# Kernel tuning notes

Measured on AMD Instinct MI355X. Metric: run time of the kernel, lower is better.

Reference implementation:

```python
import jax, jax.numpy as jnp
import numpy as np

N, E, H, FE, DIM = 50000, 800000, 128, 16, 3
MF = 2 * H + FE + 1  # message_features: 2*hidden + edge_feats + radial (e3, not relaxed)


def _lin(key, fan_in, fan_out):
    return jax.random.normal(key, (fan_in, fan_out), jnp.float32) / np.sqrt(fan_in)


def setup_inputs() -> dict:
    key = jax.random.key(0)
    ks = jax.random.split(key, 16)
    inp = {
        "h": jax.random.normal(ks[0], (N, H), jnp.float32),
        "coords": jax.random.normal(ks[1], (N, DIM), jnp.float32),
        "a": jax.random.normal(ks[2], (E, FE), jnp.float32),
        "src": jax.random.randint(ks[3], (E,), 0, N),
        "dst": jax.random.randint(ks[4], (E,), 0, N),
        # coord_mlp: Lin(MF,H)+silu, Lin(H,H)+silu, Lin(H,1,bias=False) w/ gain 0.001
        "wc1": _lin(ks[5], MF, H), "bc1": jnp.zeros((H,), jnp.float32),
        "wc2": _lin(ks[6], H, H), "bc2": jnp.zeros((H,), jnp.float32),
        "wc3": _lin(ks[7], H, 1) * 0.001,
        # edge_mlp: Lin(MF,H)+silu, Lin(H,H)+silu
        "we1": _lin(ks[8], MF, H), "be1": jnp.zeros((H,), jnp.float32),
        "we2": _lin(ks[9], H, H), "be2": jnp.zeros((H,), jnp.float32),
        # att_mlp: Lin(H,1)+sigmoid
        "wa": _lin(ks[10], H, 1), "ba": jnp.zeros((1,), jnp.float32),
        # node_mlp: Lin(2H,H)+silu, Lin(H,H)
        "wn1": _lin(ks[11], 2 * H, H), "bn1": jnp.zeros((H,), jnp.float32),
        "wn2": _lin(ks[12], H, H), "bn2": jnp.zeros((H,), jnp.float32),
    }
    return inp


def reference(h, coords, a, src, dst,
              wc1, bc1, wc2, bc2, wc3,
              we1, be1, we2, be2,
              wa, ba, wn1, bn1, wn2, bn2):
    silu = jax.nn.silu
    # --- edge gather ---
    hs, hd = h[src], h[dst]              # [E, H]
    xs, xd = coords[src], coords[dst]    # [E, 3]
    diffs = xs - xd                      # [E, 3]
    radials = jnp.sum(diffs * diffs, axis=-1, keepdims=True)  # [E, 1]
    f = jnp.concatenate([hs, hd, radials, a], axis=-1)        # [E, MF]
    # --- coord message ---
    c = silu(f @ wc1 + bc1)
    c = silu(c @ wc2 + bc2)
    scale = c @ wc3                      # [E, 1]
    msg_x = scale * diffs / (radials + 1.0)                   # [E, 3]
    # --- hidden message with attention gate ---
    m = silu(f @ we1 + be1)
    m = silu(m @ we2 + be2)              # [E, H]
    msg_h = jax.nn.sigmoid(m @ wa + ba) * m                   # [E, H]
    # --- scatter-sum to destination nodes ---
    x_agg = jax.ops.segment_sum(msg_x, dst, num_segments=N)   # [N, 3]
    h_agg = jax.ops.segment_sum(msg_h, dst, num_segments=N)   # [N, H]
    coords_out = coords + x_agg
    n = silu(jnp.concatenate([h, h_agg], axis=-1) @ wn1 + bn1)
    h_out = h + (n @ wn2 + bn2)
    return (h_out, coords_out)
```

## Files before the change

kernel.cpp:

```cpp
#include <hip/hip_runtime.h>

#define NN 50000
#define NE 800000
#define HD 128
#define FED 16
#define MFD 273
#define K1 288
#define NO1 256
#define FSTR 296
#define NFSTR 264
#define NNSTR 136

typedef __bf16 bf16x8 __attribute__((ext_vector_type(8)));
typedef float f32x4 __attribute__((ext_vector_type(4)));
typedef unsigned short u16;

__device__ __forceinline__ u16 f2b(float x) {
  unsigned u = __builtin_bit_cast(unsigned, x);
  return (u16)((u + 0x7FFFu + ((u >> 16) & 1u)) >> 16);
}
__device__ __forceinline__ float siluf(float x) { return x / (1.f + __expf(-x)); }

__global__ void pack_weights(const float* __restrict__ wc1, const float* __restrict__ we1,
                             const float* __restrict__ wc2, const float* __restrict__ we2,
                             const float* __restrict__ wn1, const float* __restrict__ wn2,
                             u16* __restrict__ W1t, u16* __restrict__ W2ct,
                             u16* __restrict__ W2mt, u16* __restrict__ Wn1t,
                             u16* __restrict__ Wn2t) {
  int i = blockIdx.x * 256 + threadIdx.x;
  if (i < 256 * K1) {
    int n = i / K1, k = i - n * K1;
    float v = 0.f;
    if (k < MFD) v = (n < HD) ? wc1[k * HD + n] : we1[k * HD + (n - HD)];
    W1t[i] = f2b(v);
    return;
  }
  int j = i - 256 * K1;
  if (j < HD * HD) {
    int n = j >> 7, k = j & 127;
    W2ct[j] = f2b(wc2[k * HD + n]);
    W2mt[j] = f2b(we2[k * HD + n]);
    return;
  }
  j -= HD * HD;
  if (j < HD * 256) {
    int n = j >> 8, k = j & 255;
    Wn1t[j] = f2b(wn1[k * HD + n]);
    return;
  }
  j -= HD * 256;
  if (j < HD * HD) {
    int n = j >> 7, k = j & 127;
    Wn2t[j] = f2b(wn2[k * HD + n]);
  }
}

__global__ __launch_bounds__(256, 2) void edge_kernel(
    const float* __restrict__ h, const float* __restrict__ coords,
    const float* __restrict__ a, const int* __restrict__ src,
    const int* __restrict__ dst,
    const float* __restrict__ bc1, const float* __restrict__ be1,
    const float* __restrict__ bc2, const float* __restrict__ be2,
    const float* __restrict__ wc3, const float* __restrict__ wa,
    const float* __restrict__ ba,
    const u16* __restrict__ W1t, const u16* __restrict__ W2ct,
    const u16* __restrict__ W2mt,
    float* __restrict__ x_agg, float* __restrict__ h_agg) {
  __shared__ u16 fL[128 * FSTR];
  __shared__ float diffL[128][3];
  __shared__ float radL[128];
  __shared__ int dstL[128];

  const int tid = threadIdx.x;
  const int wave = tid >> 6;
  const int lane = tid & 63;
  const int wrow = wave * 32;
  const int ebase = blockIdx.x * 128;

  {
    const int r = wrow + (lane >> 1);
    const int q = lane & 1;
    const int e = ebase + r;
    const int s = src[e];
    const int d = dst[e];
    const float4* hs4 = (const float4*)(h + (size_t)s * HD) + q * 16;
    const float4* hd4 = (const float4*)(h + (size_t)d * HD) + q * 16;
    u16* frow = &fL[r * FSTR];
#pragma unroll
    for (int u = 0; u < 16; ++u) {
      float4 v = hs4[u];
      ushort4 b; b.x = f2b(v.x); b.y = f2b(v.y); b.z = f2b(v.z); b.w = f2b(v.w);
      *(ushort4*)(frow + q * 64 + u * 4) = b;
    }
#pragma unroll
    for (int u = 0; u < 16; ++u) {
      float4 v = hd4[u];
      ushort4 b; b.x = f2b(v.x); b.y = f2b(v.y); b.z = f2b(v.z); b.w = f2b(v.w);
      *(ushort4*)(frow + HD + q * 64 + u * 4) = b;
    }
    if (q == 0) {
      float dx = coords[(size_t)s * 3 + 0] - coords[(size_t)d * 3 + 0];
      float dy = coords[(size_t)s * 3 + 1] - coords[(size_t)d * 3 + 1];
      float dz = coords[(size_t)s * 3 + 2] - coords[(size_t)d * 3 + 2];
      float rad = dx * dx + dy * dy + dz * dz;
      diffL[r][0] = dx; diffL[r][1] = dy; diffL[r][2] = dz;
      radL[r] = rad; dstL[r] = d;
      frow[256] = f2b(rad);
    } else {
      const float* ap = a + (size_t)e * FED;
#pragma unroll
      for (int u = 0; u < FED; ++u) frow[257 + u] = f2b(ap[u]);
#pragma unroll
      for (int u = MFD; u < K1; ++u) frow[u] = 0;
    }
  }

  const int ln = lane & 15;
  const int khi = lane >> 4;

  bf16x8 a1[2][9];
#pragma unroll
  for (int st = 0; st < 2; ++st)
#pragma unroll
    for (int kk = 0; kk < 9; ++kk)
      a1[st][kk] = *(const bf16x8*)&fL[(wrow + st * 16 + ln) * FSTR + kk * 32 + khi * 8];

#pragma unroll 2
  for (int nt = 0; nt < 16; ++nt) {
    const int col = nt * 16 + ln;
    const float b0 = (col < HD) ? bc1[col] : be1[col - HD];
    f32x4 acc0 = {b0, b0, b0, b0};
    f32x4 acc1 = {b0, b0, b0, b0};
    const u16* wp = &W1t[(size_t)col * K1];
#pragma unroll
    for (int kk = 0; kk < 9; ++kk) {
      bf16x8 bf = *(const bf16x8*)(wp + kk * 32 + khi * 8);
      acc0 = __builtin_amdgcn_mfma_f32_16x16x32_bf16(a1[0][kk], bf, acc0, 0, 0, 0);
      acc1 = __builtin_amdgcn_mfma_f32_16x16x32_bf16(a1[1][kk], bf, acc1, 0, 0, 0);
    }
#pragma unroll
    for (int i = 0; i < 4; ++i) {
      fL[(wrow + khi * 4 + i) * FSTR + col] = f2b(siluf(acc0[i]));
      fL[(wrow + 16 + khi * 4 + i) * FSTR + col] = f2b(siluf(acc1[i]));
    }
  }

  bf16x8 a2c[2][4], a2m[2][4];
#pragma unroll
  for (int st = 0; st < 2; ++st)
#pragma unroll
    for (int kk = 0; kk < 4; ++kk) {
      a2c[st][kk] = *(const bf16x8*)&fL[(wrow + st * 16 + ln) * FSTR + kk * 32 + khi * 8];
      a2m[st][kk] = *(const bf16x8*)&fL[(wrow + st * 16 + ln) * FSTR + HD + kk * 32 + khi * 8];
    }

  f32x4 m2s0[8], m2s1[8];
  f32x4 pscale0 = {0, 0, 0, 0}, pscale1 = {0, 0, 0, 0};
  f32x4 patt0 = {0, 0, 0, 0}, patt1 = {0, 0, 0, 0};
#pragma unroll
  for (int nt = 0; nt < 8; ++nt) {
    const int col = nt * 16 + ln;
    const float w3 = wc3[col];
    const float wav = wa[col];
    const float bc2v = bc2[col];
    const float be2v = be2[col];
    f32x4 ac0 = {bc2v, bc2v, bc2v, bc2v}, ac1 = {bc2v, bc2v, bc2v, bc2v};
    f32x4 am0 = {be2v, be2v, be2v, be2v}, am1 = {be2v, be2v, be2v, be2v};
    const u16* wpc = &W2ct[(size_t)col * HD];
    const u16* wpm = &W2mt[(size_t)col * HD];
#pragma unroll
    for (int kk = 0; kk < 4; ++kk) {
      bf16x8 bc = *(const bf16x8*)(wpc + kk * 32 + khi * 8);
      bf16x8 bm = *(const bf16x8*)(wpm + kk * 32 + khi * 8);
      ac0 = __builtin_amdgcn_mfma_f32_16x16x32_bf16(a2c[0][kk], bc, ac0, 0, 0, 0);
      ac1 = __builtin_amdgcn_mfma_f32_16x16x32_bf16(a2c[1][kk], bc, ac1, 0, 0, 0);
      am0 = __builtin_amdgcn_mfma_f32_16x16x32_bf16(a2m[0][kk], bm, am0, 0, 0, 0);
      am1 = __builtin_amdgcn_mfma_f32_16x16x32_bf16(a2m[1][kk], bm, am1, 0, 0, 0);
    }
#pragma unroll
    for (int i = 0; i < 4; ++i) {
      float c0 = siluf(ac0[i]); pscale0[i] += c0 * w3;
      float c1 = siluf(ac1[i]); pscale1[i] += c1 * w3;
      float m0 = siluf(am0[i]); patt0[i] += m0 * wav; am0[i] = m0;
      float m1 = siluf(am1[i]); patt1[i] += m1 * wav; am1[i] = m1;
    }
    m2s0[nt] = am0;
    m2s1[nt] = am1;
  }

#pragma unroll
  for (int off = 1; off < 16; off <<= 1) {
#pragma unroll
    for (int i = 0; i < 4; ++i) {
      pscale0[i] += __shfl_xor(pscale0[i], off);
      pscale1[i] += __shfl_xor(pscale1[i], off);
      patt0[i] += __shfl_xor(patt0[i], off);
      patt1[i] += __shfl_xor(patt1[i], off);
    }
  }

  if (ln < 3) {
#pragma unroll
    for (int i = 0; i < 4; ++i) {
      int r0 = wrow + khi * 4 + i;
      int r1 = r0 + 16;
      float v0 = pscale0[i] * diffL[r0][ln] / (radL[r0] + 1.f);
      float v1 = pscale1[i] * diffL[r1][ln] / (radL[r1] + 1.f);
      atomicAdd(&x_agg[(size_t)dstL[r0] * 3 + ln], v0);
      atomicAdd(&x_agg[(size_t)dstL[r1] * 3 + ln], v1);
    }
  }

  const float bav = ba[0];
  f32x4 att0, att1;
  size_t hb0[4], hb1[4];
#pragma unroll
  for (int i = 0; i < 4; ++i) {
    att0[i] = 1.f / (1.f + __expf(-(patt0[i] + bav)));
    att1[i] = 1.f / (1.f + __expf(-(patt1[i] + bav)));
    hb0[i] = (size_t)dstL[wrow + khi * 4 + i] * HD;
    hb1[i] = (size_t)dstL[wrow + 16 + khi * 4 + i] * HD;
  }
#pragma unroll
  for (int nt = 0; nt < 8; ++nt) {
    const int col = nt * 16 + ln;
#pragma unroll
    for (int i = 0; i < 4; ++i) {
      atomicAdd(&h_agg[hb0[i] + col], att0[i] * m2s0[nt][i]);
      atomicAdd(&h_agg[hb1[i] + col], att1[i] * m2s1[nt][i]);
    }
  }
}

__global__ __launch_bounds__(256, 2) void node_kernel(
    const float* __restrict__ h, const float* __restrict__ coords,
    const float* __restrict__ bn1, const float* __restrict__ bn2,
    const u16* __restrict__ Wn1t, const u16* __restrict__ Wn2t,
    const float* __restrict__ x_agg, const float* __restrict__ h_agg,
    float* __restrict__ out) {
  __shared__ u16 fL[64 * NFSTR];
  __shared__ u16 nL[64 * NNSTR];
  const int tid = threadIdx.x;
  const int wave = tid >> 6;
  const int lane = tid & 63;
  const int nbase = blockIdx.x * 64;

  if (tid < 192) {
    int idx = nbase * 3 + tid;
    if (idx < NN * 3) out[(size_t)NN * HD + idx] = coords[idx] + x_agg[idx];
  }

  const int wrow = wave * 16;
  {
    const int r = wrow + (lane >> 2);
    const int q = lane & 3;
    const int node = nbase + r;
    const int nn = (node < NN) ? node : 0;
    const float4* hp = (const float4*)(h + (size_t)nn * HD) + q * 8;
    const float4* gp = (const float4*)(h_agg + (size_t)nn * HD) + q * 8;
    u16* frow = &fL[r * NFSTR];
#pragma unroll
    for (int u = 0; u < 8; ++u) {
      float4 v = hp[u];
      ushort4 b; b.x = f2b(v.x); b.y = f2b(v.y); b.z = f2b(v.z); b.w = f2b(v.w);
      *(ushort4*)(frow + q * 32 + u * 4) = b;
      float4 w = gp[u];
      ushort4 c; c.x = f2b(w.x); c.y = f2b(w.y); c.z = f2b(w.z); c.w = f2b(w.w);
      *(ushort4*)(frow + HD + q * 32 + u * 4) = c;
    }
  }

  const int ln = lane & 15;
  const int khi = lane >> 4;

  bf16x8 a1[8];
#pragma unroll
  for (int kk = 0; kk < 8; ++kk)
    a1[kk] = *(const bf16x8*)&fL[(wrow + ln) * NFSTR + kk * 32 + khi * 8];

#pragma unroll 2
  for (int nt = 0; nt < 8; ++nt) {
    const int col = nt * 16 + ln;
    const float b = bn1[col];
    f32x4 acc = {b, b, b, b};
    const u16* wp = &Wn1t[(size_t)col * 256];
#pragma unroll
    for (int kk = 0; kk < 8; ++kk) {
      bf16x8 bf = *(const bf16x8*)(wp + kk * 32 + khi * 8);
      acc = __builtin_amdgcn_mfma_f32_16x16x32_bf16(a1[kk], bf, acc, 0, 0, 0);
    }
#pragma unroll
    for (int i = 0; i < 4; ++i)
      nL[(wrow + khi * 4 + i) * NNSTR + col] = f2b(siluf(acc[i]));
  }

  bf16x8 a2[4];
#pragma unroll
  for (int kk = 0; kk < 4; ++kk)
    a2[kk] = *(const bf16x8*)&nL[(wrow + ln) * NNSTR + kk * 32 + khi * 8];

#pragma unroll 2
  for (int nt = 0; nt < 8; ++nt) {
    const int col = nt * 16 + ln;
    const float b = bn2[col];
    f32x4 acc = {b, b, b, b};
    const u16* wp = &Wn2t[(size_t)col * HD];
#pragma unroll
    for (int kk = 0; kk < 4; ++kk) {
      bf16x8 bf = *(const bf16x8*)(wp + kk * 32 + khi * 8);
      acc = __builtin_amdgcn_mfma_f32_16x16x32_bf16(a2[kk], bf, acc, 0, 0, 0);
    }
#pragma unroll
    for (int i = 0; i < 4; ++i) {
      const int node = nbase + wrow + khi * 4 + i;
      if (node < NN)
        out[(size_t)node * HD + col] = h[(size_t)node * HD + col] + acc[i];
    }
  }
}

extern "C" void kernel_launch(void* const* d_in, const int* in_sizes, int n_in,
                              void* d_out, int out_size, void* d_ws, size_t ws_size,
                              hipStream_t stream) {
  const float* h = (const float*)d_in[0];
  const float* coords = (const float*)d_in[1];
  const float* a = (const float*)d_in[2];
  const int* src = (const int*)d_in[3];
  const int* dst = (const int*)d_in[4];
  const float* wc1 = (const float*)d_in[5];
  const float* bc1 = (const float*)d_in[6];
  const float* wc2 = (const float*)d_in[7];
  const float* bc2 = (const float*)d_in[8];
  const float* wc3 = (const float*)d_in[9];
  const float* we1 = (const float*)d_in[10];
  const float* be1 = (const float*)d_in[11];
  const float* we2 = (const float*)d_in[12];
  const float* be2 = (const float*)d_in[13];
  const float* wa = (const float*)d_in[14];
  const float* ba = (const float*)d_in[15];
  const float* wn1 = (const float*)d_in[16];
  const float* bn1 = (const float*)d_in[17];
  const float* wn2 = (const float*)d_in[18];
  const float* bn2 = (const float*)d_in[19];
  float* out = (float*)d_out;

  char* ws = (char*)d_ws;
  const size_t OFF_XAGG = 0;
  const size_t OFF_HAGG = 600064;
  const size_t OFF_W1T = 26200064;
  const size_t OFF_W2CT = 26347520;
  const size_t OFF_W2MT = 26380288;
  const size_t OFF_WN1T = 26413056;
  const size_t OFF_WN2T = 26478592;

  float* x_agg = (float*)(ws + OFF_XAGG);
  float* h_agg = (float*)(ws + OFF_HAGG);
  u16* W1t = (u16*)(ws + OFF_W1T);
  u16* W2ct = (u16*)(ws + OFF_W2CT);
  u16* W2mt = (u16*)(ws + OFF_W2MT);
  u16* Wn1t = (u16*)(ws + OFF_WN1T);
  u16* Wn2t = (u16*)(ws + OFF_WN2T);

  (void)hipMemsetAsync(ws, 0, OFF_W1T, stream);

  pack_weights<<<544, 256, 0, stream>>>(wc1, we1, wc2, we2, wn1, wn2,
                                        W1t, W2ct, W2mt, Wn1t, Wn2t);

  edge_kernel<<<NE / 128, 256, 0, stream>>>(h, coords, a, src, dst,
                                            bc1, be1, bc2, be2, wc3, wa, ba,
                                            W1t, W2ct, W2mt, x_agg, h_agg);

  node_kernel<<<(NN + 63) / 64, 256, 0, stream>>>(h, coords, bn1, bn2,
                                                  Wn1t, Wn2t, x_agg, h_agg, out);
}
```

Baseline: 995.0 us.

## Sort edges by destination and segment-reduce messages before scattering to h_agg

Adds a counting sort of edges by destination (histogram, single-block scan, atomic scatter into a permutation). The edge kernel then processes edges in sorted order, stages the gated hidden messages in reused shared memory, and reduces runs of equal destinations within each wave. A run is written with a plain store when it lies entirely inside the wave, and with an atomic add only at wave boundaries. This is meant to remove most of the per-element float atomics into h_agg. The cost is three extra preprocessing kernels and less regular gathers of the a array through the permutation. The a-feature load is also vectorized to float4.

Result: slower. 1.052 ms (+5.7%).

```diff
diff --git a/kernel.cpp b/kernel.cpp
--- a/kernel.cpp
+++ b/kernel.cpp
@@ -6,8 +6,8 @@
 #define FED 16
 #define MFD 273
 #define K1 288
-#define NO1 256
 #define FSTR 296
+#define GSTR 132
 #define NFSTR 264
 #define NNSTR 136
 
@@ -55,10 +55,56 @@
   }
 }
 
+__global__ void hist_kernel(const int* __restrict__ dst, int* __restrict__ cnt) {
+  int i = blockIdx.x * 256 + threadIdx.x;
+  if (i < NE) atomicAdd(&cnt[dst[i]], 1);
+}
+
+#define SCAN_T 1024
+#define SCAN_CHUNK 49
+__global__ __launch_bounds__(SCAN_T) void scan_kernel(const int* __restrict__ cnt,
+                                                      int* __restrict__ offs) {
+  __shared__ int ps[SCAN_T];
+  const int t = threadIdx.x;
+  const int base = t * SCAN_CHUNK;
+  int s = 0;
+#pragma unroll
+  for (int j = 0; j < SCAN_CHUNK; ++j) {
+    int idx = base + j;
+    s += (idx < NN) ? cnt[idx] : 0;
+  }
+  ps[t] = s;
+  __syncthreads();
+  for (int off = 1; off < SCAN_T; off <<= 1) {
+    int v = (t >= off) ? ps[t - off] : 0;
+    __syncthreads();
+    ps[t] += v;
+    __syncthreads();
+  }
+  int run = (t == 0) ? 0 : ps[t - 1];
+  for (int j = 0; j < SCAN_CHUNK; ++j) {
+    int idx = base + j;
+    if (idx < NN) {
+      offs[idx] = run;
+      run += cnt[idx];
+    }
+  }
+}
+
+__global__ void scatter_kernel(const int* __restrict__ dst, int* __restrict__ offs,
+                               int* __restrict__ perm) {
+  int e = blockIdx.x * 256 + threadIdx.x;
+  if (e < NE) {
+    int d = dst[e];
+    int p = atomicAdd(&offs[d], 1);
+    perm[p] = e;
+  }
+}
+
 __global__ __launch_bounds__(256, 2) void edge_kernel(
     const float* __restrict__ h, const float* __restrict__ coords,
     const float* __restrict__ a, const int* __restrict__ src,
-    const int* __restrict__ dst,
+    const int* __restrict__ dst, const int* __restrict__ perm,
     const float* __restrict__ bc1, const float* __restrict__ be1,
     const float* __restrict__ bc2, const float* __restrict__ be2,
     const float* __restrict__ wc3, const float* __restrict__ wa,
@@ -66,21 +112,23 @@
     const u16* __restrict__ W1t, const u16* __restrict__ W2ct,
     const u16* __restrict__ W2mt,
     float* __restrict__ x_agg, float* __restrict__ h_agg) {
-  __shared__ u16 fL[128 * FSTR];
+  __shared__ __align__(16) unsigned char smem[128 * FSTR * 2];
   __shared__ float diffL[128][3];
   __shared__ float radL[128];
   __shared__ int dstL[128];
+  u16* fL = (u16*)smem;
 
   const int tid = threadIdx.x;
   const int wave = tid >> 6;
   const int lane = tid & 63;
   const int wrow = wave * 32;
   const int ebase = blockIdx.x * 128;
+  float* gw = (float*)(smem + (size_t)wave * (32 * FSTR * 2));
 
   {
     const int r = wrow + (lane >> 1);
     const int q = lane & 1;
-    const int e = ebase + r;
+    const int e = perm[ebase + r];
     const int s = src[e];
     const int d = dst[e];
     const float4* hs4 = (const float4*)(h + (size_t)s * HD) + q * 16;
@@ -107,9 +155,15 @@
       radL[r] = rad; dstL[r] = d;
       frow[256] = f2b(rad);
     } else {
-      const float* ap = a + (size_t)e * FED;
-#pragma unroll
-      for (int u = 0; u < FED; ++u) frow[257 + u] = f2b(ap[u]);
+      const float4* ap4 = (const float4*)(a + (size_t)e * FED);
+#pragma unroll
+      for (int u = 0; u < 4; ++u) {
+        float4 v = ap4[u];
+        frow[257 + u * 4 + 0] = f2b(v.x);
+        frow[257 + u * 4 + 1] = f2b(v.y);
+        frow[257 + u * 4 + 2] = f2b(v.z);
+        frow[257 + u * 4 + 3] = f2b(v.w);
+      }
 #pragma unroll
       for (int u = MFD; u < K1; ++u) frow[u] = 0;
     }
@@ -213,22 +267,42 @@
 
   const float bav = ba[0];
   f32x4 att0, att1;
-  size_t hb0[4], hb1[4];
 #pragma unroll
   for (int i = 0; i < 4; ++i) {
     att0[i] = 1.f / (1.f + __expf(-(patt0[i] + bav)));
     att1[i] = 1.f / (1.f + __expf(-(patt1[i] + bav)));
-    hb0[i] = (size_t)dstL[wrow + khi * 4 + i] * HD;
-    hb1[i] = (size_t)dstL[wrow + 16 + khi * 4 + i] * HD;
   }
 #pragma unroll
   for (int nt = 0; nt < 8; ++nt) {
     const int col = nt * 16 + ln;
 #pragma unroll
     for (int i = 0; i < 4; ++i) {
-      atomicAdd(&h_agg[hb0[i] + col], att0[i] * m2s0[nt][i]);
-      atomicAdd(&h_agg[hb1[i] + col], att1[i] * m2s1[nt][i]);
-    }
+      gw[(khi * 4 + i) * GSTR + col] = att0[i] * m2s0[nt][i];
+      gw[(16 + khi * 4 + i) * GSTR + col] = att1[i] * m2s1[nt][i];
+    }
+  }
+
+  const int gbase = ebase + wrow;
+  const int prevd = (gbase == 0) ? -1 : dst[perm[gbase - 1]];
+  const int nextd = (gbase + 32 >= NE) ? -1 : dst[perm[gbase + 32]];
+
+#pragma unroll
+  for (int cc = 0; cc < 2; ++cc) {
+    const int c = lane + cc * 64;
+    float acc = 0.f;
+    int cur = dstL[wrow];
+    bool open_start = (cur == prevd);
+    for (int r = 0; r < 32; ++r) {
+      int dr = dstL[wrow + r];
+      if (dr != cur) {
+        if (open_start) atomicAdd(&h_agg[(size_t)cur * HD + c], acc);
+        else h_agg[(size_t)cur * HD + c] = acc;
+        acc = 0.f; cur = dr; open_start = false;
+      }
+      acc += gw[r * GSTR + c];
+    }
+    if (open_start || cur == nextd) atomicAdd(&h_agg[(size_t)cur * HD + c], acc);
+    else h_agg[(size_t)cur * HD + c] = acc;
   }
 }
 
@@ -347,26 +421,36 @@
   char* ws = (char*)d_ws;
   const size_t OFF_XAGG = 0;
   const size_t OFF_HAGG = 600064;
-  const size_t OFF_W1T = 26200064;
-  const size_t OFF_W2CT = 26347520;
-  const size_t OFF_W2MT = 26380288;
-  const size_t OFF_WN1T = 26413056;
-  const size_t OFF_WN2T = 26478592;
+  const size_t OFF_CNT = 26200064;
+  const size_t MEMSET_BYTES = 26400256;
+  const size_t OFF_OFFS = 26400256;
+  const size_t OFF_PERM = 26600448;
+  const size_t OFF_W1T = 29800448;
+  const size_t OFF_W2CT = 29947904;
+  const size_t OFF_W2MT = 29980672;
+  const size_t OFF_WN1T = 30013440;
+  const size_t OFF_WN2T = 30078976;
 
   float* x_agg = (float*)(ws + OFF_XAGG);
   float* h_agg = (float*)(ws + OFF_HAGG);
+  int* cnt = (int*)(ws + OFF_CNT);
+  int* offs = (int*)(ws + OFF_OFFS);
+  int* perm = (int*)(ws + OFF_PERM);
   u16* W1t = (u16*)(ws + OFF_W1T);
   u16* W2ct = (u16*)(ws + OFF_W2CT);
   u16* W2mt = (u16*)(ws + OFF_W2MT);
   u16* Wn1t = (u16*)(ws + OFF_WN1T);
   u16* Wn2t = (u16*)(ws + OFF_WN2T);
 
-  (void)hipMemsetAsync(ws, 0, OFF_W1T, stream);
+  (void)hipMemsetAsync(ws, 0, MEMSET_BYTES, stream);
 
   pack_weights<<<544, 256, 0, stream>>>(wc1, we1, wc2, we2, wn1, wn2,
                                         W1t, W2ct, W2mt, Wn1t, Wn2t);
-
-  edge_kernel<<<NE / 128, 256, 0, stream>>>(h, coords, a, src, dst,
+  hist_kernel<<<(NE + 255) / 256, 256, 0, stream>>>(dst, cnt);
+  scan_kernel<<<1, SCAN_T, 0, stream>>>(cnt, offs);
+  scatter_kernel<<<(NE + 255) / 256, 256, 0, stream>>>(dst, offs, perm);
+
+  edge_kernel<<<NE / 128, 256, 0, stream>>>(h, coords, a, src, dst, perm,
                                             bc1, be1, bc2, be2, wc3, wa, ba,
                                             W1t, W2ct, W2mt, x_agg, h_agg);
 
```
